# Kernel tuning notes

Measured on AMD Instinct MI355X. Metric: run time of the kernel, lower is better.

Reference implementation:

```python
import jax, jax.numpy as jnp
import numpy as np

N_NODES = 100000


def _spmm(edge_index, edge_weight, x):
    # out[i] = sum_j A[i, j] * x[j]; row=dst=edge_index[0], col=src=edge_index[1]
    dst, src = edge_index[0], edge_index[1]
    msgs = edge_weight[:, None] * x[src]  # [E, d]
    return jax.ops.segment_sum(msgs, dst, num_segments=N_NODES)


def setup_inputs() -> dict:
    key = jax.random.key(0)
    k1, k2, k3, k4 = jax.random.split(key, 4)
    N, E, D = N_NODES, 3200000, 64
    features = jax.random.normal(k1, (N, D), dtype=jnp.float32)
    edge_weight = jax.random.uniform(k2, (E,), dtype=jnp.float32)
    dst = jax.random.randint(k3, (E,), 0, N)
    src = jax.random.randint(k4, (E,), 0, N)
    edge_index = jnp.stack([dst, src]).astype(jnp.int64)
    return {"features": features, "edge_weight": edge_weight,
            "edge_index": edge_index, "degree": 2}


def reference(features, edge_weight, edge_index, degree):
    # SGC: features = adj @ features, repeated `degree` times (no learned params)
    x = features
    for _ in range(degree):
        x = _spmm(edge_index, edge_weight, x)
    return x
```

## Files before the change

### kernel.cpp

```cpp
#include <hip/hip_runtime.h>
#include <hip/hip_fp16.h>

#define N_NODES 100000
#define DFEAT 64
#define CH 4096
#define NBK 782
#define NPB 128
#define CAPB 4608

__device__ __forceinline__ void scan2_1024(int v0, int v1, int* sb, int tid,
                                           int* e0, int* e1, int* total)
{
    __syncthreads();
    const int lane = tid & 63, wid = tid >> 6;
    int s = v0 + v1;
    int inc = s;
#pragma unroll
    for (int o = 1; o < 64; o <<= 1) {
        int t = __shfl_up(inc, o, 64);
        if (lane >= o) inc += t;
    }
    if (lane == 63) sb[wid] = inc;
    __syncthreads();
    if (wid == 0) {
        int wv = (lane < 8) ? sb[lane] : 0;
        int winc = wv;
#pragma unroll
        for (int o = 1; o < 8; o <<= 1) {
            int t = __shfl_up(winc, o, 64);
            if (lane >= o) winc += t;
        }
        if (lane < 8) sb[8 + lane] = winc - wv;
    }
    __syncthreads();
    int base = sb[8 + wid] + inc - s;
    *e0 = base;
    *e1 = base + v0;
    *total = sb[15] + sb[7];
}

__global__ __launch_bounds__(512) void sort_chunks(
    const int* __restrict__ dst, const int* __restrict__ src,
    const float* __restrict__ w,
    unsigned* __restrict__ recs_g, unsigned char* __restrict__ dloc_g,
    int* __restrict__ off_T, int E, int nch,
    const float* __restrict__ feat_in, __half* __restrict__ feat_out, int n2)
{
    __shared__ int  hist[NBK + 1];
    __shared__ int  cursor[NBK];
    __shared__ int  sb[16];
    __shared__ unsigned      lrec[CH];
    __shared__ unsigned char ldl[CH];

    const int chunk = blockIdx.x;
    const int base  = chunk * CH;
    const int n     = min(CH, E - base);
    const int tid   = threadIdx.x;

    for (int i = tid; i < NBK + 1; i += 512) hist[i] = 0;
    __syncthreads();

    for (int k = tid; k < n; k += 512) atomicAdd(&hist[dst[base + k] >> 7], 1);

    const int i0 = 2 * tid, i1 = 2 * tid + 1;
    int v0 = 0, v1 = 0;
    __syncthreads();
    v0 = (i0 < NBK) ? hist[i0] : 0;
    v1 = (i1 < NBK) ? hist[i1] : 0;
    int e0, e1, tot;
    scan2_1024(v0, v1, sb, tid, &e0, &e1, &tot);
    if (i0 <= NBK) off_T[(size_t)i0 * nch + chunk] = base + e0;
    if (i1 <= NBK) off_T[(size_t)i1 * nch + chunk] = base + e1;
    if (i0 < NBK) cursor[i0] = e0;
    if (i1 < NBK) cursor[i1] = e1;
    __syncthreads();

    for (int k = tid; k < n; k += 512) {
        int d = dst[base + k];
        int pos = atomicAdd(&cursor[d >> 7], 1);
        unsigned wq = (unsigned)__float2int_rn(w[base + k] * 32768.0f);
        if (wq > 32767u) wq = 32767u;
        lrec[pos] = (unsigned)src[base + k] | (wq << 17);
        ldl[pos]  = (unsigned char)(d & 127);
    }
    __syncthreads();

    int4* rg = (int4*)(recs_g + base);
    const int4* rl = (const int4*)lrec;
    for (int k = tid; k < ((n + 3) >> 2); k += 512) rg[k] = rl[k];
    int4* dg = (int4*)(dloc_g + base);
    const int4* dl4 = (const int4*)ldl;
    for (int k = tid; k < ((n + 15) >> 4); k += 512) dg[k] = dl4[k];

    const int gstride = gridDim.x * 512;
    for (int i = blockIdx.x * 512 + tid; i < n2; i += gstride) {
        float2 f = ((const float2*)feat_in)[i];
        ((__half2*)feat_out)[i] = __floats2half2_rn(f.x, f.y);
    }
}

__global__ __launch_bounds__(512) void build_csr(
    const int* __restrict__ off_T, const unsigned* __restrict__ recs_g,
    const unsigned char* __restrict__ dloc_g,
    unsigned* __restrict__ edges_s, int* __restrict__ row_ptr,
    int nch, int E, int scan_const)
{
    __shared__ unsigned      lrecL[CAPB];
    __shared__ unsigned char dlocL[CAPB];
    __shared__ int gsrcL[NBK];
    __shared__ int ldstL[NBK];
    __shared__ int histL[NPB];
    __shared__ int cursorL[NPB];
    __shared__ int sb[16];

    const int b   = blockIdx.x;
    const int tid = threadIdx.x;

    const int c0 = 2 * tid, c1 = c0 + 1;
    int a00 = 0, a01 = 0, l0 = 0, l1 = 0;
    if (c0 < nch) {
        a00 = off_T[(size_t)b * nch + c0];
        int a1 = off_T[(size_t)(b + 1) * nch + c0];
        gsrcL[c0] = a00;
        l0 = a1 - a00;
    }
    if (c1 < nch) {
        a01 = off_T[(size_t)b * nch + c1];
        int a1 = off_T[(size_t)(b + 1) * nch + c1];
        gsrcL[c1] = a01;
        l1 = a1 - a01;
    }

    int ra, rb_, rowsum;
    scan2_1024(a00, a01, sb, tid, &ra, &rb_, &rowsum);
    const int gb = rowsum - scan_const;

    int d0, d1, cnt;
    scan2_1024(l0, l1, sb, tid, &d0, &d1, &cnt);
    if (c0 < nch) ldstL[c0] = d0;
    if (c1 < nch) ldstL[c1] = d1;
    if (tid < NPB) histL[tid] = 0;
    __syncthreads();

    const int cntC = min(cnt, CAPB);

#pragma unroll
    for (int j = 0; j < (CAPB + 511) / 512; ++j) {
        int k = tid + j * 512;
        if (k < cntC) {
            int lo = 0, hi = nch;
            while (hi - lo > 1) {
                int mid = (lo + hi) >> 1;
                if (ldstL[mid] <= k) lo = mid; else hi = mid;
            }
            int sp = gsrcL[lo] + (k - ldstL[lo]);
            lrecL[k] = recs_g[sp];
            dlocL[k] = dloc_g[sp];
        }
    }
    __syncthreads();

    for (int k = tid; k < cntC; k += 512) atomicAdd(&histL[dlocL[k]], 1);
    __syncthreads();

    int h0 = (2 * tid < NPB) ? histL[2 * tid] : 0;
    int h1 = (2 * tid + 1 < NPB) ? histL[2 * tid + 1] : 0;
    int he0, he1, htot;
    scan2_1024(h0, h1, sb, tid, &he0, &he1, &htot);
    if (2 * tid < NPB) {
        int i = b * NPB + 2 * tid;
        if (i < N_NODES) row_ptr[i] = gb + he0;
        cursorL[2 * tid] = gb + he0;
    }
    if (2 * tid + 1 < NPB) {
        int i = b * NPB + 2 * tid + 1;
        if (i < N_NODES) row_ptr[i] = gb + he1;
        cursorL[2 * tid + 1] = gb + he1;
    }
    if (b == NBK - 1 && tid == 0) row_ptr[N_NODES] = E;
    __syncthreads();

    for (int k = tid; k < cntC; k += 512) {
        int pos = atomicAdd(&cursorL[dlocL[k]], 1);
        edges_s[pos] = lrecL[k];
    }
}

template <int OUT_FP16>
__global__ __launch_bounds__(256) void spmm_csr(
    const int* __restrict__ row_ptr,
    const unsigned* __restrict__ edges,
    const uint2* __restrict__ x4,
    void* __restrict__ outv)
{
    int node = __builtin_amdgcn_readfirstlane(blockIdx.x * 4 + (int)(threadIdx.x >> 6));
    if (node >= N_NODES) return;
    const int lane = threadIdx.x & 63;
    const int g    = lane >> 4;
    const int gl   = lane & 15;

    const int beg = row_ptr[node];
    const int end = row_ptr[node + 1];

    float a0 = 0.f, a1 = 0.f, a2 = 0.f, a3 = 0.f;
    int e0 = beg;
    const int nblk = (end - beg) >> 4;

#define ACC4(v, w) do {                                            \
        __half2 _h0 = *(__half2*)&(v).x;                           \
        __half2 _h1 = *(__half2*)&(v).y;                           \
        a0 += (w) * __low2float(_h0);  a1 += (w) * __high2float(_h0); \
        a2 += (w) * __low2float(_h1);  a3 += (w) * __high2float(_h1); \
    } while (0)

    if (nblk > 0) {
        unsigned n0 = edges[e0 +  0 + g];
        unsigned n1 = edges[e0 +  4 + g];
        unsigned n2 = edges[e0 +  8 + g];
        unsigned n3 = edges[e0 + 12 + g];
        e0 += 16;

        for (int b = 0; b < nblk; ++b) {
            uint2 v0 = x4[(size_t)(n0 & 0x1FFFF) * 16 + gl];
            uint2 v1 = x4[(size_t)(n1 & 0x1FFFF) * 16 + gl];
            uint2 v2 = x4[(size_t)(n2 & 0x1FFFF) * 16 + gl];
            uint2 v3 = x4[(size_t)(n3 & 0x1FFFF) * 16 + gl];

            float w0 = (float)(n0 >> 17), w1 = (float)(n1 >> 17);
            float w2 = (float)(n2 >> 17), w3 = (float)(n3 >> 17);

            if (b + 1 < nblk) {
                n0 = edges[e0 +  0 + g];
                n1 = edges[e0 +  4 + g];
                n2 = edges[e0 +  8 + g];
                n3 = edges[e0 + 12 + g];
                e0 += 16;
            }

            ACC4(v0, w0);
            ACC4(v1, w1);
            ACC4(v2, w2);
            ACC4(v3, w3);
        }
    }

    for (; e0 + 4 <= end; e0 += 4) {
        unsigned r = edges[e0 + g];
        uint2 v = x4[(size_t)(r & 0x1FFFF) * 16 + gl];
        float w = (float)(r >> 17);
        ACC4(v, w);
    }
    {
        int rem = end - e0;
        if (g < rem) {
            unsigned r = edges[e0 + g];
            uint2 v = x4[(size_t)(r & 0x1FFFF) * 16 + gl];
            float w = (float)(r >> 17);
            ACC4(v, w);
        }
    }
#undef ACC4

    a0 += __shfl_xor(a0, 16, 64);  a0 += __shfl_xor(a0, 32, 64);
    a1 += __shfl_xor(a1, 16, 64);  a1 += __shfl_xor(a1, 32, 64);
    a2 += __shfl_xor(a2, 16, 64);  a2 += __shfl_xor(a2, 32, 64);
    a3 += __shfl_xor(a3, 16, 64);  a3 += __shfl_xor(a3, 32, 64);

    if (g == 0) {
        const float k = 1.0f / 32768.0f;
        float s0 = a0 * k, s1 = a1 * k, s2 = a2 * k, s3 = a3 * k;
        if (OUT_FP16) {
            __half2 p0 = __floats2half2_rn(s0, s1);
            __half2 p1 = __floats2half2_rn(s2, s3);
            uint2 pv;
            pv.x = *(unsigned*)&p0;
            pv.y = *(unsigned*)&p1;
            ((uint2*)outv)[(size_t)node * 16 + gl] = pv;
        } else {
            ((float4*)outv)[(size_t)node * 16 + gl] = make_float4(s0, s1, s2, s3);
        }
    }
}

extern "C" void kernel_launch(void* const* d_in, const int* in_sizes, int n_in,
                              void* d_out, int out_size, void* d_ws, size_t ws_size,
                              hipStream_t stream) {
    const float* features = (const float*)d_in[0];
    const float* edge_w   = (const float*)d_in[1];
    const int*   edge_idx = (const int*)d_in[2];

    const int E = in_sizes[1];
    const int* dst = edge_idx;
    const int* src = edge_idx + E;

    const int nch = (E + CH - 1) / CH;

    char* ws = (char*)d_ws;
    unsigned*      recs_g  = (unsigned*)ws;      ws += (size_t)nch * CH * sizeof(unsigned);
    unsigned char* dloc_g  = (unsigned char*)ws; ws += (size_t)nch * CH;
    unsigned*      edges_s = (unsigned*)ws;      ws += (size_t)E * sizeof(unsigned);
    __half*        feat_h  = (__half*)ws;        ws += (size_t)N_NODES * DFEAT * sizeof(__half);
    int*           off_T   = (int*)ws;           ws += (size_t)(NBK + 1) * nch * sizeof(int);
    int*           row_ptr = (int*)ws;           ws += (size_t)(N_NODES + 1) * sizeof(int);

    __half* tmp_h = (__half*)recs_g;

    float* out = (float*)d_out;

    const int scan_const = (int)((long long)CH * (((long long)(nch - 1) * nch) / 2));

    const int n2 = N_NODES * DFEAT / 2;

    sort_chunks<<<nch, 512, 0, stream>>>(dst, src, edge_w, recs_g, dloc_g, off_T,
                                         E, nch, features, feat_h, n2);
    build_csr  <<<NBK, 512, 0, stream>>>(off_T, recs_g, dloc_g, edges_s, row_ptr,
                                         nch, E, scan_const);

    const int ngrid = (N_NODES + 3) / 4;
    spmm_csr<1><<<ngrid, 256, 0, stream>>>(row_ptr, edges_s, (const uint2*)feat_h, tmp_h);
    spmm_csr<0><<<ngrid, 256, 0, stream>>>(row_ptr, edges_s, (const uint2*)tmp_h, out);
}
```

Before: 262.9 us.

## Replace chunk-sorted offsets with global atomic bucket append for CSR build

The old two-pass chunk sort (per-chunk histogram, a transposed offset table, then a binary search per edge in the build step) is replaced by a scheme where each block reserves space in fixed-capacity global buckets through padded global atomics and scatters records straight into them. A single-block scan computes bucket bases, and the finalize kernel reads contiguous bucket data with no binary search. This removes the off_T table and the search cost, but the scatter writes are now uncoalesced across buckets and two extra small launches are added. Buckets hold at most CAPB entries, so an overflowing bucket would write past its slot.

```diff
diff --git a/kernel.cpp b/kernel.cpp
--- a/kernel.cpp
+++ b/kernel.cpp
@@ -7,6 +7,7 @@
 #define NBK 782
 #define NPB 128
 #define CAPB 4608
+#define CPAD 16
 
 __device__ __forceinline__ void scan2_1024(int v0, int v1, int* sb, int tid,
                                            int* e0, int* e1, int* total)
@@ -39,58 +40,52 @@
     *total = sb[15] + sb[7];
 }
 
-__global__ __launch_bounds__(512) void sort_chunks(
+__global__ __launch_bounds__(512) void zero_cnt(int* __restrict__ gcur)
+{
+    int i = blockIdx.x * 512 + threadIdx.x;
+    if (i < NBK * CPAD) gcur[i] = 0;
+}
+
+__global__ __launch_bounds__(512) void bucket_append(
     const int* __restrict__ dst, const int* __restrict__ src,
     const float* __restrict__ w,
-    unsigned* __restrict__ recs_g, unsigned char* __restrict__ dloc_g,
-    int* __restrict__ off_T, int E, int nch,
+    int* __restrict__ gcur,
+    unsigned* __restrict__ recs_b,
+    unsigned char* __restrict__ dloc_b,
+    int E,
     const float* __restrict__ feat_in, __half* __restrict__ feat_out, int n2)
 {
-    __shared__ int  hist[NBK + 1];
-    __shared__ int  cursor[NBK];
-    __shared__ int  sb[16];
-    __shared__ unsigned      lrec[CH];
-    __shared__ unsigned char ldl[CH];
-
-    const int chunk = blockIdx.x;
-    const int base  = chunk * CH;
-    const int n     = min(CH, E - base);
-    const int tid   = threadIdx.x;
-
-    for (int i = tid; i < NBK + 1; i += 512) hist[i] = 0;
+    __shared__ int hist[NBK];
+    __shared__ int cursL[NBK];
+    __shared__ int baseL[NBK];
+    __shared__ int sb[16];
+
+    const int base = blockIdx.x * CH;
+    const int n    = min(CH, E - base);
+    const int tid  = threadIdx.x;
+
+    for (int i = tid; i < NBK; i += 512) { hist[i] = 0; cursL[i] = 0; }
     __syncthreads();
 
     for (int k = tid; k < n; k += 512) atomicAdd(&hist[dst[base + k] >> 7], 1);
-
-    const int i0 = 2 * tid, i1 = 2 * tid + 1;
-    int v0 = 0, v1 = 0;
-    __syncthreads();
-    v0 = (i0 < NBK) ? hist[i0] : 0;
-    v1 = (i1 < NBK) ? hist[i1] : 0;
-    int e0, e1, tot;
-    scan2_1024(v0, v1, sb, tid, &e0, &e1, &tot);
-    if (i0 <= NBK) off_T[(size_t)i0 * nch + chunk] = base + e0;
-    if (i1 <= NBK) off_T[(size_t)i1 * nch + chunk] = base + e1;
-    if (i0 < NBK) cursor[i0] = e0;
-    if (i1 < NBK) cursor[i1] = e1;
+    __syncthreads();
+
+    for (int i = tid; i < NBK; i += 512) {
+        int h = hist[i];
+        baseL[i] = h ? atomicAdd(&gcur[i * CPAD], h) : 0;
+    }
     __syncthreads();
 
     for (int k = tid; k < n; k += 512) {
         int d = dst[base + k];
-        int pos = atomicAdd(&cursor[d >> 7], 1);
+        int b = d >> 7;
+        int pos = baseL[b] + atomicAdd(&cursL[b], 1);
         unsigned wq = (unsigned)__float2int_rn(w[base + k] * 32768.0f);
         if (wq > 32767u) wq = 32767u;
-        lrec[pos] = (unsigned)src[base + k] | (wq << 17);
-        ldl[pos]  = (unsigned char)(d & 127);
-    }
-    __syncthreads();
-
-    int4* rg = (int4*)(recs_g + base);
-    const int4* rl = (const int4*)lrec;
-    for (int k = tid; k < ((n + 3) >> 2); k += 512) rg[k] = rl[k];
-    int4* dg = (int4*)(dloc_g + base);
-    const int4* dl4 = (const int4*)ldl;
-    for (int k = tid; k < ((n + 15) >> 4); k += 512) dg[k] = dl4[k];
+        size_t gp = (size_t)b * CAPB + pos;
+        recs_b[gp] = (unsigned)src[base + k] | (wq << 17);
+        dloc_b[gp] = (unsigned char)(d & 127);
+    }
 
     const int gstride = gridDim.x * 512;
     for (int i = blockIdx.x * 512 + tid; i < n2; i += gstride) {
@@ -99,68 +94,49 @@
     }
 }
 
-__global__ __launch_bounds__(512) void build_csr(
-    const int* __restrict__ off_T, const unsigned* __restrict__ recs_g,
-    const unsigned char* __restrict__ dloc_g,
-    unsigned* __restrict__ edges_s, int* __restrict__ row_ptr,
-    int nch, int E, int scan_const)
+__global__ __launch_bounds__(512) void scan_buckets(
+    const int* __restrict__ gcur, int* __restrict__ gbase,
+    int* __restrict__ row_ptr, int E)
+{
+    __shared__ int sb[16];
+    const int tid = threadIdx.x;
+    const int i0 = 2 * tid, i1 = 2 * tid + 1;
+    int v0 = (i0 < NBK) ? gcur[i0 * CPAD] : 0;
+    int v1 = (i1 < NBK) ? gcur[i1 * CPAD] : 0;
+    int e0, e1, tot;
+    scan2_1024(v0, v1, sb, tid, &e0, &e1, &tot);
+    if (i0 < NBK) gbase[i0] = e0;
+    if (i1 < NBK) gbase[i1] = e1;
+    if (tid == 0) row_ptr[N_NODES] = E;
+}
+
+__global__ __launch_bounds__(512) void finalize_csr(
+    const int* __restrict__ gcur, const int* __restrict__ gbase,
+    const unsigned* __restrict__ recs_b, const unsigned char* __restrict__ dloc_b,
+    unsigned* __restrict__ edges_s, int* __restrict__ row_ptr)
 {
     __shared__ unsigned      lrecL[CAPB];
     __shared__ unsigned char dlocL[CAPB];
-    __shared__ int gsrcL[NBK];
-    __shared__ int ldstL[NBK];
     __shared__ int histL[NPB];
     __shared__ int cursorL[NPB];
     __shared__ int sb[16];
 
     const int b   = blockIdx.x;
     const int tid = threadIdx.x;
-
-    const int c0 = 2 * tid, c1 = c0 + 1;
-    int a00 = 0, a01 = 0, l0 = 0, l1 = 0;
-    if (c0 < nch) {
-        a00 = off_T[(size_t)b * nch + c0];
-        int a1 = off_T[(size_t)(b + 1) * nch + c0];
-        gsrcL[c0] = a00;
-        l0 = a1 - a00;
-    }
-    if (c1 < nch) {
-        a01 = off_T[(size_t)b * nch + c1];
-        int a1 = off_T[(size_t)(b + 1) * nch + c1];
-        gsrcL[c1] = a01;
-        l1 = a1 - a01;
-    }
-
-    int ra, rb_, rowsum;
-    scan2_1024(a00, a01, sb, tid, &ra, &rb_, &rowsum);
-    const int gb = rowsum - scan_const;
-
-    int d0, d1, cnt;
-    scan2_1024(l0, l1, sb, tid, &d0, &d1, &cnt);
-    if (c0 < nch) ldstL[c0] = d0;
-    if (c1 < nch) ldstL[c1] = d1;
+    const int cnt = gcur[b * CPAD];
+    const int gb  = gbase[b];
+
     if (tid < NPB) histL[tid] = 0;
     __syncthreads();
 
-    const int cntC = min(cnt, CAPB);
-
-#pragma unroll
-    for (int j = 0; j < (CAPB + 511) / 512; ++j) {
-        int k = tid + j * 512;
-        if (k < cntC) {
-            int lo = 0, hi = nch;
-            while (hi - lo > 1) {
-                int mid = (lo + hi) >> 1;
-                if (ldstL[mid] <= k) lo = mid; else hi = mid;
-            }
-            int sp = gsrcL[lo] + (k - ldstL[lo]);
-            lrecL[k] = recs_g[sp];
-            dlocL[k] = dloc_g[sp];
-        }
-    }
-    __syncthreads();
-
-    for (int k = tid; k < cntC; k += 512) atomicAdd(&histL[dlocL[k]], 1);
+    const size_t rb = (size_t)b * CAPB;
+    for (int k = tid; k < cnt; k += 512) {
+        lrecL[k] = recs_b[rb + k];
+        dlocL[k] = dloc_b[rb + k];
+    }
+    __syncthreads();
+
+    for (int k = tid; k < cnt; k += 512) atomicAdd(&histL[dlocL[k]], 1);
     __syncthreads();
 
     int h0 = (2 * tid < NPB) ? histL[2 * tid] : 0;
@@ -177,10 +153,9 @@
         if (i < N_NODES) row_ptr[i] = gb + he1;
         cursorL[2 * tid + 1] = gb + he1;
     }
-    if (b == NBK - 1 && tid == 0) row_ptr[N_NODES] = E;
-    __syncthreads();
-
-    for (int k = tid; k < cntC; k += 512) {
+    __syncthreads();
+
+    for (int k = tid; k < cnt; k += 512) {
         int pos = atomicAdd(&cursorL[dlocL[k]], 1);
         edges_s[pos] = lrecL[k];
     }
@@ -293,28 +268,28 @@
     const int* dst = edge_idx;
     const int* src = edge_idx + E;
 
-    const int nch = (E + CH - 1) / CH;
+    const int nblkK1 = (E + CH - 1) / CH;
 
     char* ws = (char*)d_ws;
-    unsigned*      recs_g  = (unsigned*)ws;      ws += (size_t)nch * CH * sizeof(unsigned);
-    unsigned char* dloc_g  = (unsigned char*)ws; ws += (size_t)nch * CH;
+    unsigned*      recs_b  = (unsigned*)ws;      ws += (size_t)NBK * CAPB * sizeof(unsigned);
+    unsigned char* dloc_b  = (unsigned char*)ws; ws += (size_t)NBK * CAPB;
     unsigned*      edges_s = (unsigned*)ws;      ws += (size_t)E * sizeof(unsigned);
     __half*        feat_h  = (__half*)ws;        ws += (size_t)N_NODES * DFEAT * sizeof(__half);
-    int*           off_T   = (int*)ws;           ws += (size_t)(NBK + 1) * nch * sizeof(int);
+    int*           gcur    = (int*)ws;           ws += (size_t)NBK * CPAD * sizeof(int);
+    int*           gbase   = (int*)ws;           ws += (size_t)NBK * sizeof(int);
     int*           row_ptr = (int*)ws;           ws += (size_t)(N_NODES + 1) * sizeof(int);
 
-    __half* tmp_h = (__half*)recs_g;
+    __half* tmp_h = (__half*)recs_b;
 
     float* out = (float*)d_out;
 
-    const int scan_const = (int)((long long)CH * (((long long)(nch - 1) * nch) / 2));
-
     const int n2 = N_NODES * DFEAT / 2;
 
-    sort_chunks<<<nch, 512, 0, stream>>>(dst, src, edge_w, recs_g, dloc_g, off_T,
-                                         E, nch, features, feat_h, n2);
-    build_csr  <<<NBK, 512, 0, stream>>>(off_T, recs_g, dloc_g, edges_s, row_ptr,
-                                         nch, E, scan_const);
+    zero_cnt     <<<(NBK * CPAD + 511) / 512, 512, 0, stream>>>(gcur);
+    bucket_append<<<nblkK1, 512, 0, stream>>>(dst, src, edge_w, gcur, recs_b, dloc_b,
+                                              E, features, feat_h, n2);
+    scan_buckets <<<1, 512, 0, stream>>>(gcur, gbase, row_ptr, E);
+    finalize_csr <<<NBK, 512, 0, stream>>>(gcur, gbase, recs_b, dloc_b, edges_s, row_ptr);
 
     const int ngrid = (N_NODES + 3) / 4;
     spmm_csr<1><<<ngrid, 256, 0, stream>>>(row_ptr, edges_s, (const uint2*)feat_h, tmp_h);
```

Measured after the change: 353.3 us. +34.4%, slower.
